# Optimization experiments

Hardware: AMD Instinct MI355X
Metric: run time of the kernel (lower is better)

The kernel has to match this reference:

```python
import jax, jax.numpy as jnp
import numpy as np

EPS = 1e-5

def _layer_norm(y, w, b):
    mu = y.mean(-1, keepdims=True)
    var = jnp.mean((y - mu) ** 2, axis=-1, keepdims=True)
    return (y - mu) * jax.lax.rsqrt(var + EPS) * w + b


def setup_inputs() -> dict:
    key = jax.random.key(0)
    ks = jax.random.split(key, 8)
    B, D, H, W = 1, 96, 96, 96
    N, R, K = 16, 6, 4
    x = jax.random.normal(ks[0], (B, D, H, W), jnp.float32)
    x_proj_weight = jax.random.normal(ks[1], (K, R + 2 * N, D), jnp.float32) * 0.05
    dt_projs_weight = jax.random.normal(ks[2], (K, D, R), jnp.float32) * 0.1
    dt_projs_bias = jax.random.normal(ks[3], (K, D), jnp.float32) * 0.1
    A_logs = jax.random.normal(ks[4], (K * D, N), jnp.float32)
    Ds = jax.random.normal(ks[5], (K * D,), jnp.float32) * 0.1
    ln_w = jnp.ones((D,), jnp.float32)
    ln_b = jnp.zeros((D,), jnp.float32)
    return {"x": x, "x_proj_weight": x_proj_weight, "dt_projs_weight": dt_projs_weight,
            "dt_projs_bias": dt_projs_bias, "A_logs": A_logs, "Ds": Ds,
            "ln_w": ln_w, "ln_b": ln_b}


def reference(x, x_proj_weight, dt_projs_weight, dt_projs_bias, A_logs, Ds, ln_w, ln_b):
    B, D, H, W = x.shape
    L = H * W
    K = x_proj_weight.shape[0]            # 4 scan directions
    N = A_logs.shape[1]                   # d_state
    R = dt_projs_weight.shape[2]          # dt_rank

    # ---- CrossScan: 4 directional flattenings -> xs [B, K, D, L]
    xs0 = x.reshape(B, D, L)
    xs1 = jnp.swapaxes(x, 2, 3).reshape(B, D, L)
    xs = jnp.stack([xs0, xs1, xs0[:, :, ::-1], xs1[:, :, ::-1]], axis=1)

    # ---- input-dependent projections
    x_dbl = jnp.einsum('bkdl,kcd->bkcl', xs, x_proj_weight)    # [B,K,R+2N,L]
    dts = x_dbl[:, :, :R]
    Bs = x_dbl[:, :, R:R + N]                                  # [B,K,N,L]
    Cs = x_dbl[:, :, R + N:]                                   # [B,K,N,L]
    dts = jnp.einsum('bkrl,kdr->bkdl', dts, dt_projs_weight)   # [B,K,D,L]

    # ---- selective scan (S6), delta_softplus=True, fp32
    delta = jax.nn.softplus(dts + dt_projs_bias[None, :, :, None])   # [B,K,D,L]
    A = -jnp.exp(A_logs).reshape(K, D, N)                             # [K,D,N]
    dA = jnp.exp(jnp.einsum('bkdl,kdn->bkdln', delta, A))             # [B,K,D,L,N]
    dBu = jnp.einsum('bkdl,bknl,bkdl->bkdln', delta, Bs, xs)          # delta*B*u

    def combine(c1, c2):
        a1, b1 = c1
        a2, b2 = c2
        return a1 * a2, a2 * b1 + b2

    _, h = jax.lax.associative_scan(combine, (dA, dBu), axis=3)       # h_t over L

    y = jnp.einsum('bkdln,bknl->bkdl', h, Cs)
    y = y + xs * Ds.reshape(K, D)[None, :, :, None]                   # [B,K,D,L]

    # ---- CrossMerge: undo the 4 directional scans and sum
    ys = y[:, 0:2] + y[:, 2:4, :, ::-1]                               # [B,2,D,L]
    ym = ys[:, 0] + jnp.swapaxes(ys[:, 1].reshape(B, D, W, H), 2, 3).reshape(B, D, L)

    # ---- out_norm (LayerNorm over D) and reshape to [B,H,W,D]
    yout = jnp.swapaxes(ym, 1, 2)                                     # [B,L,D]
    yout = _layer_norm(yout, ln_w, ln_b).reshape(B, H, W, D)
    return yout.astype(x.dtype)
```

## Files before the change

### kernel.cpp

```cpp
#include <hip/hip_runtime.h>
#include <math.h>

constexpr int cD = 96, cL = 9216, cK = 4;
constexpr int CL = 36, NCH = 256;
constexpr long cDL = (long)cD * cL;
constexpr float LOG2E = 1.44269504088896f;

constexpr long OFF_XT    = 0;
constexpr long OFF_DELTA = OFF_XT    + cDL;
constexpr long OFF_BC    = OFF_DELTA + 4L*cDL;
constexpr long OFF_Y     = OFF_BC    + 4L*cL*32;
constexpr long OFF_YT    = OFF_Y     + 4L*cDL;

__device__ __forceinline__ float4 a2prep(float4 v) {
    return make_float4(-LOG2E * exp2f(LOG2E * v.x), -LOG2E * exp2f(LOG2E * v.y),
                       -LOG2E * exp2f(LOG2E * v.z), -LOG2E * exp2f(LOG2E * v.w));
}
template<int C>
__device__ __forceinline__ float qperm(float v) {
    return __int_as_float(__builtin_amdgcn_mov_dpp(__float_as_int(v), C, 0xf, 0xf, true));
}

__global__ __launch_bounds__(256) void kT(const float* __restrict__ x,
                                          float* __restrict__ xT) {
    __shared__ float t[32][33];
    const int h0 = blockIdx.x * 32, w0 = blockIdx.y * 32, d = blockIdx.z;
    const float* xd = x + (long)d * cL;
    float* xtd = xT + (long)d * cL;
    for (int o = threadIdx.x; o < 1024; o += 256) {
        int i = o >> 5, j = o & 31;
        t[i][j] = xd[(h0 + i) * 96 + w0 + j];
    }
    __syncthreads();
    for (int o = threadIdx.x; o < 1024; o += 256) {
        int i = o >> 5, j = o & 31;
        xtd[(w0 + i) * 96 + h0 + j] = t[j][i];
    }
}

__global__ __launch_bounds__(256) void kA(const float* __restrict__ x,
                                          const float* __restrict__ xT,
                                          const float* __restrict__ xpw,
                                          const float* __restrict__ dtw,
                                          const float* __restrict__ dtb,
                                          float* __restrict__ delta,
                                          float* __restrict__ BC) {
    __shared__ float xs[96][64];
    __shared__ float xdbl[38][65];
    __shared__ float dtw_l[96 * 6];
    __shared__ float dtb_l[96];
    const int p0 = blockIdx.x * 64;
    const int k  = blockIdx.y;
    const int tid = threadIdx.x;
    const float* src = (k & 1) ? xT : x;

    for (int o = tid; o < 96 * 64; o += 256) {
        int dd = o >> 6, pp = o & 63;
        xs[dd][pp] = src[(long)dd * cL + p0 + pp];
    }
    for (int o = tid; o < 96 * 6; o += 256) dtw_l[o] = dtw[k * 96 * 6 + o];
    if (tid < 96) dtb_l[tid] = dtb[k * 96 + tid];
    __syncthreads();

    const int lane = tid & 63;
    const int c0 = __builtin_amdgcn_readfirstlane((tid >> 6) * 10);
    const float* wk = xpw + (long)k * 38 * 96;
    float acc[10];
    #pragma unroll
    for (int i = 0; i < 10; ++i) acc[i] = 0.f;
    #pragma unroll 4
    for (int dd = 0; dd < 96; ++dd) {
        float xv = xs[dd][lane];
        #pragma unroll
        for (int i = 0; i < 10; ++i) {
            int c = c0 + i; c = c > 37 ? 37 : c;
            acc[i] = fmaf(xv, wk[c * 96 + dd], acc[i]);
        }
    }
    #pragma unroll
    for (int i = 0; i < 10; ++i) {
        int c = c0 + i; c = c > 37 ? 37 : c;
        xdbl[c][lane] = acc[i];
    }
    __syncthreads();

    for (int o = tid; o < 64 * 16; o += 256) {
        int n = o & 15, pp = o >> 4;
        int P = p0 + pp;
        int q = (k < 2) ? P : (9215 - P);
        int ch = q / 36, j = q - ch * 36;
        long idx = (((long)k * 36 + j) * 256 + ch) * 32 + n;
        BC[idx]      = xdbl[6 + n][pp];
        BC[idx + 16] = xdbl[22 + n][pp];
    }
    for (int o = tid; o < 96 * 64; o += 256) {
        int dd = o >> 6, pp = o & 63;
        float s = dtb_l[dd];
        #pragma unroll
        for (int r = 0; r < 6; ++r) s = fmaf(xdbl[r][pp], dtw_l[dd * 6 + r], s);
        float sp = fmaxf(s, 0.f) + __logf(1.f + __expf(-fabsf(s)));
        delta[((long)(k * 96 + dd)) * cL + p0 + pp] = sp;
    }
}

__global__ __launch_bounds__(1024, 2) void kS(const float* __restrict__ x,
                                              const float* __restrict__ xT,
                                              const float* __restrict__ delta,
                                              const float* __restrict__ BC,
                                              const float* __restrict__ Alog,
                                              const float* __restrict__ Dsv,
                                              float* __restrict__ y) {
    __shared__ float lp[NCH][16];
    __shared__ float ls[NCH][16];
    float* gpf = &lp[0][0];
    const int tid = threadIdx.x;
    const int seq = blockIdx.x;
    const int k = seq / 96, d = seq % 96, rev = k >> 1;
    const int n0 = (tid & 3) * 4, ch = tid >> 2;
    const int r = tid & 3;
    const int q0 = rev ? (9215 - ch * CL) : ch * CL;

    const float4 a2 = a2prep(*(const float4*)(Alog + (long)seq * 16 + n0));
    const float Dv = Dsv[seq];
    const float* dB = delta + (long)seq * cL + q0;
    const float* xB = ((k & 1) ? xT : x) + (long)d * cL + q0;
    const float* bcB = BC + (long)k * cL * 32 + (long)ch * 32 + n0;

    float4 h = make_float4(0.f, 0.f, 0.f, 0.f);
    float sdl = 0.f;
#define S1(DL, XV, OFF) { \
        float4 B = *(const float4*)(bcB + (OFF) * 8192); \
        float t = (DL) * (XV); sdl += (DL); \
        h.x = fmaf(exp2f((DL)*a2.x), h.x, t*B.x); \
        h.y = fmaf(exp2f((DL)*a2.y), h.y, t*B.y); \
        h.z = fmaf(exp2f((DL)*a2.z), h.z, t*B.z); \
        h.w = fmaf(exp2f((DL)*a2.w), h.w, t*B.w); }
    if (!rev) {
        #pragma unroll
        for (int g = 0; g < 9; ++g) {
            float4 d4 = *(const float4*)(dB + 4*g);
            float4 x4 = *(const float4*)(xB + 4*g);
            S1(d4.x, x4.x, 4*g)   S1(d4.y, x4.y, 4*g+1)
            S1(d4.z, x4.z, 4*g+2) S1(d4.w, x4.w, 4*g+3)
        }
    } else {
        #pragma unroll
        for (int g = 0; g < 9; ++g) {
            float4 d4 = *(const float4*)(dB - 4*g - 3);
            float4 x4 = *(const float4*)(xB - 4*g - 3);
            S1(d4.w, x4.w, 4*g)   S1(d4.z, x4.z, 4*g+1)
            S1(d4.y, x4.y, 4*g+2) S1(d4.x, x4.x, 4*g+3)
        }
    }
#undef S1
    *(float4*)&lp[ch][n0] = make_float4(exp2f(a2.x*sdl), exp2f(a2.y*sdl),
                                        exp2f(a2.z*sdl), exp2f(a2.w*sdl));
    *(float4*)&ls[ch][n0] = h;
    __syncthreads();

    const int sn = tid & 15, sg = tid >> 4;
    float LPe[4], LSe[4];
    {
        float P = 1.f, S = 0.f;
        #pragma unroll
        for (int i = 0; i < 4; ++i) {
            LPe[i] = P; LSe[i] = S;
            float p = lp[sg * 4 + i][sn], s = ls[sg * 4 + i][sn];
            S = fmaf(p, S, s); P = p * P;
        }
        __syncthreads();
        gpf[tid] = P; gpf[1024 + tid] = S;
    }
    __syncthreads();
    #pragma unroll
    for (int off = 1; off < 64; off <<= 1) {
        float pc = gpf[tid], sc = gpf[1024 + tid];
        float pn = pc, snn = sc;
        if (sg >= off) {
            pn  = pc * gpf[tid - off * 16];
            snn = fmaf(pc, gpf[1024 + tid - off * 16], sc);
        }
        __syncthreads();
        gpf[tid] = pn; gpf[1024 + tid] = snn;
        __syncthreads();
    }
    const float GS = (sg == 0) ? 0.f : gpf[1024 + tid - 16];
    #pragma unroll
    for (int i = 0; i < 4; ++i) ls[sg * 4 + i][sn] = fmaf(LPe[i], GS, LSe[i]);
    __syncthreads();

    h = *(float4*)&ls[ch][n0];
    float* yq = y + (long)seq * cL + ch * CL;
    float yhold = 0.f;
#define S2(DL, XV, SI, OFF) { \
        float4 B = *(const float4*)(bcB + (OFF) * 8192); \
        float4 C = *(const float4*)(bcB + (OFF) * 8192 + 16); \
        float t = (DL) * (XV); \
        h.x = fmaf(exp2f((DL)*a2.x), h.x, t*B.x); \
        h.y = fmaf(exp2f((DL)*a2.y), h.y, t*B.y); \
        h.z = fmaf(exp2f((DL)*a2.z), h.z, t*B.z); \
        h.w = fmaf(exp2f((DL)*a2.w), h.w, t*B.w); \
        float pv = fmaf(h.x, C.x, fmaf(h.y, C.y, fmaf(h.z, C.z, h.w * C.w))); \
        pv += qperm<0xB1>(pv); \
        pv += qperm<0x4E>(pv); \
        if ((SI) == r) yhold = fmaf(Dv, (XV), pv); }
    if (!rev) {
        #pragma unroll
        for (int g = 0; g < 9; ++g) {
            float4 d4 = *(const float4*)(dB + 4*g);
            float4 x4 = *(const float4*)(xB + 4*g);
            S2(d4.x, x4.x, 0, 4*g)   S2(d4.y, x4.y, 1, 4*g+1)
            S2(d4.z, x4.z, 2, 4*g+2) S2(d4.w, x4.w, 3, 4*g+3)
            yq[4*g + r] = yhold;
        }
    } else {
        #pragma unroll
        for (int g = 0; g < 9; ++g) {
            float4 d4 = *(const float4*)(dB - 4*g - 3);
            float4 x4 = *(const float4*)(xB - 4*g - 3);
            S2(d4.w, x4.w, 0, 4*g)   S2(d4.z, x4.z, 1, 4*g+1)
            S2(d4.y, x4.y, 2, 4*g+2) S2(d4.x, x4.x, 3, 4*g+3)
            yq[4*g + r] = yhold;
        }
    }
#undef S2
}

__global__ __launch_bounds__(256) void kU(const float* __restrict__ Y,
                                          float* __restrict__ YT) {
    __shared__ float t[32][33];
    const int i0 = blockIdx.x * 32, j0 = blockIdx.y * 32;
    const int z = blockIdx.z;
    const int arr = z / 96, d = z % 96;
    const float* src = Y + (1 + 2 * arr) * cDL + (long)d * cL;
    float* dst = YT + (long)arr * cDL + (long)d * cL;
    for (int o = threadIdx.x; o < 1024; o += 256) {
        int i = o >> 5, j = o & 31;
        t[i][j] = src[(i0 + i) * 96 + j0 + j];
    }
    __syncthreads();
    for (int o = threadIdx.x; o < 1024; o += 256) {
        int i = o >> 5, j = o & 31;
        dst[(j0 + i) * 96 + i0 + j] = t[j][i];
    }
}

__global__ __launch_bounds__(256) void kE(const float* __restrict__ Y,
                                          const float* __restrict__ YT,
                                          const float* __restrict__ lnw,
                                          const float* __restrict__ lnb,
                                          float* __restrict__ out) {
    __shared__ float vs[96][36];
    __shared__ float red[8][32], red2[8][32];
    __shared__ float MU[32], RS[32];
    const int tid = threadIdx.x;
    const int p0 = blockIdx.x * 32;

    for (int o = tid; o < 96 * 8; o += 256) {
        int dd = o >> 3, j = o & 7;
        const float* r0 = Y + (long)dd * cL + p0;
        const float* r1 = YT + (long)dd * cL + p0;
        const float* r2 = Y + 2 * cDL + (long)dd * cL;
        const float* r3 = YT + cDL + (long)dd * cL;
        float4 a = ((const float4*)r0)[j];
        float4 b = ((const float4*)r1)[j];
        float4 c = *(const float4*)(r2 + 9212 - p0 - 4 * j);
        float4 e = *(const float4*)(r3 + 9212 - p0 - 4 * j);
        *(float4*)&vs[dd][4 * j] = make_float4(a.x + b.x + c.w + e.w,
                                               a.y + b.y + c.z + e.z,
                                               a.z + b.z + c.y + e.y,
                                               a.w + b.w + c.x + e.x);
    }
    __syncthreads();

    const int p = tid & 31, part = tid >> 5;
    float s = 0.f, s2 = 0.f;
    for (int dd = part * 12; dd < part * 12 + 12; ++dd) {
        float v = vs[dd][p];
        s += v; s2 = fmaf(v, v, s2);
    }
    red[part][p] = s; red2[part][p] = s2;
    __syncthreads();
    if (tid < 32) {
        float S = 0.f, S2 = 0.f;
        #pragma unroll
        for (int q = 0; q < 8; ++q) { S += red[q][tid]; S2 += red2[q][tid]; }
        float m = S * (1.f / 96.f);
        MU[tid] = m;
        RS[tid] = rsqrtf(S2 * (1.f / 96.f) - m * m + 1e-5f);
    }
    __syncthreads();
    for (int o = tid; o < 32 * 96; o += 256) {
        int pl = o / 96, dd = o - pl * 96;
        out[(long)(p0 + pl) * 96 + dd] = (vs[dd][pl] - MU[pl]) * RS[pl] * lnw[dd] + lnb[dd];
    }
}

extern "C" void kernel_launch(void* const* d_in, const int* in_sizes, int n_in,
                              void* d_out, int out_size, void* d_ws, size_t ws_size,
                              hipStream_t stream) {
    const float* x    = (const float*)d_in[0];
    const float* xpw  = (const float*)d_in[1];
    const float* dtw  = (const float*)d_in[2];
    const float* dtb  = (const float*)d_in[3];
    const float* Alog = (const float*)d_in[4];
    const float* Dsv  = (const float*)d_in[5];
    const float* lnw  = (const float*)d_in[6];
    const float* lnb  = (const float*)d_in[7];
    float* ws = (float*)d_ws;

    float* xT    = ws + OFF_XT;
    float* delta = ws + OFF_DELTA;
    float* BC    = ws + OFF_BC;
    float* y     = ws + OFF_Y;
    float* yT    = ws + OFF_YT;
    float* out   = (float*)d_out;

    kT<<<dim3(3, 3, 96), 256, 0, stream>>>(x, xT);
    kA<<<dim3(144, 4), 256, 0, stream>>>(x, xT, xpw, dtw, dtb, delta, BC);
    kS<<<cK * cD, 1024, 0, stream>>>(x, xT, delta, BC, Alog, Dsv, y);
    kU<<<dim3(3, 3, 192), 256, 0, stream>>>(y, yT);
    kE<<<288, 256, 0, stream>>>(y, yT, lnw, lnb, out);
}
```

Measured before the change: 113.6 us.

## Split chunked selective scan into two kernels with half-sequence blocks

Replaces the single 1024-thread scan kernel with two kernels. The first computes per-chunk decay products and partial states into global buffers. The second reloads all chunk summaries, redoes the cross-chunk prefix, and runs the output pass, each block covering half of a sequence's chunks. The point is more, smaller blocks (768 × 512 threads with higher occupancy bounds) to better fill the GPU. The B/C buffer is also reordered so each group of four timesteps sits contiguously per chunk. The costs are an extra launch, a global round trip for chunk summaries, and a prefix computed redundantly by both halves.

```diff
diff --git a/kernel.cpp b/kernel.cpp
--- a/kernel.cpp
+++ b/kernel.cpp
@@ -11,6 +11,8 @@
 constexpr long OFF_BC    = OFF_DELTA + 4L*cDL;
 constexpr long OFF_Y     = OFF_BC    + 4L*cL*32;
 constexpr long OFF_YT    = OFF_Y     + 4L*cDL;
+constexpr long OFF_PG    = OFF_YT    + 2L*cDL;
+constexpr long OFF_SG    = OFF_PG    + 384L*256*16;
 
 __device__ __forceinline__ float4 a2prep(float4 v) {
     return make_float4(-LOG2E * exp2f(LOG2E * v.x), -LOG2E * exp2f(LOG2E * v.y),
@@ -89,7 +91,8 @@
         int P = p0 + pp;
         int q = (k < 2) ? P : (9215 - P);
         int ch = q / 36, j = q - ch * 36;
-        long idx = (((long)k * 36 + j) * 256 + ch) * 32 + n;
+        int g = j >> 2, r = j & 3;
+        long idx = ((((long)k * 9 + g) * 256 + ch) * 4 + r) * 32 + n;
         BC[idx]      = xdbl[6 + n][pp];
         BC[idx + 16] = xdbl[22 + n][pp];
     }
@@ -103,98 +106,126 @@
     }
 }
 
-__global__ __launch_bounds__(1024, 2) void kS(const float* __restrict__ x,
+__global__ __launch_bounds__(512, 6) void kS1(const float* __restrict__ x,
+                                              const float* __restrict__ xT,
+                                              const float* __restrict__ delta,
+                                              const float* __restrict__ BC,
+                                              const float* __restrict__ Alog,
+                                              float* __restrict__ Pg,
+                                              float* __restrict__ Sg) {
+    const int tid = threadIdx.x;
+    const int n0 = (tid & 3) * 4, chl = tid >> 2;
+    const int hb = blockIdx.x & 1, seq = blockIdx.x >> 1;
+    const int k = seq / 96, d = seq % 96, rev = k >> 1;
+    const int ch = hb * 128 + chl;
+    const int q0 = ch * CL;
+
+    const float4 a2 = a2prep(*(const float4*)(Alog + (long)seq * 16 + n0));
+    const float* dRow = delta + (long)seq * cL;
+    const float* xRow = ((k & 1) ? xT : x) + (long)d * cL;
+    const float* bc0 = BC + ((long)k * 9 * 256 * 4 + (long)ch * 4) * 32 + n0;
+
+    float4 h = make_float4(0.f, 0.f, 0.f, 0.f);
+    float sdl = 0.f;
+#define ST(DL, XV, BPTR, ROFF) { \
+        float4 B = *(const float4*)((BPTR) + (ROFF) * 32); \
+        float t = (DL) * (XV); sdl += (DL); \
+        h.x = fmaf(exp2f((DL)*a2.x), h.x, t*B.x); \
+        h.y = fmaf(exp2f((DL)*a2.y), h.y, t*B.y); \
+        h.z = fmaf(exp2f((DL)*a2.z), h.z, t*B.z); \
+        h.w = fmaf(exp2f((DL)*a2.w), h.w, t*B.w); }
+    #pragma unroll
+    for (int g = 0; g < 9; ++g) {
+        const float* bg = bc0 + (long)g * 32768;
+        if (!rev) {
+            float4 d4 = *(const float4*)(dRow + q0 + 4 * g);
+            float4 x4 = *(const float4*)(xRow + q0 + 4 * g);
+            ST(d4.x, x4.x, bg, 0) ST(d4.y, x4.y, bg, 1)
+            ST(d4.z, x4.z, bg, 2) ST(d4.w, x4.w, bg, 3)
+        } else {
+            float4 d4 = *(const float4*)(dRow + 9212 - q0 - 4 * g);
+            float4 x4 = *(const float4*)(xRow + 9212 - q0 - 4 * g);
+            ST(d4.w, x4.w, bg, 0) ST(d4.z, x4.z, bg, 1)
+            ST(d4.y, x4.y, bg, 2) ST(d4.x, x4.x, bg, 3)
+        }
+    }
+#undef ST
+    long o = ((long)seq * NCH + ch) * 16 + n0;
+    *(float4*)(Pg + o) = make_float4(exp2f(a2.x*sdl), exp2f(a2.y*sdl),
+                                     exp2f(a2.z*sdl), exp2f(a2.w*sdl));
+    *(float4*)(Sg + o) = h;
+}
+
+__global__ __launch_bounds__(512, 6) void kS2(const float* __restrict__ x,
                                               const float* __restrict__ xT,
                                               const float* __restrict__ delta,
                                               const float* __restrict__ BC,
                                               const float* __restrict__ Alog,
                                               const float* __restrict__ Dsv,
+                                              const float* __restrict__ Pg,
+                                              const float* __restrict__ Sg,
                                               float* __restrict__ y) {
     __shared__ float lp[NCH][16];
     __shared__ float ls[NCH][16];
     float* gpf = &lp[0][0];
     const int tid = threadIdx.x;
-    const int seq = blockIdx.x;
+    const int hb = blockIdx.x & 1, seq = blockIdx.x >> 1;
     const int k = seq / 96, d = seq % 96, rev = k >> 1;
-    const int n0 = (tid & 3) * 4, ch = tid >> 2;
-    const int r = tid & 3;
-    const int q0 = rev ? (9215 - ch * CL) : ch * CL;
-
-    const float4 a2 = a2prep(*(const float4*)(Alog + (long)seq * 16 + n0));
-    const float Dv = Dsv[seq];
-    const float* dB = delta + (long)seq * cL + q0;
-    const float* xB = ((k & 1) ? xT : x) + (long)d * cL + q0;
-    const float* bcB = BC + (long)k * cL * 32 + (long)ch * 32 + n0;
-
-    float4 h = make_float4(0.f, 0.f, 0.f, 0.f);
-    float sdl = 0.f;
-#define S1(DL, XV, OFF) { \
-        float4 B = *(const float4*)(bcB + (OFF) * 8192); \
-        float t = (DL) * (XV); sdl += (DL); \
-        h.x = fmaf(exp2f((DL)*a2.x), h.x, t*B.x); \
-        h.y = fmaf(exp2f((DL)*a2.y), h.y, t*B.y); \
-        h.z = fmaf(exp2f((DL)*a2.z), h.z, t*B.z); \
-        h.w = fmaf(exp2f((DL)*a2.w), h.w, t*B.w); }
-    if (!rev) {
-        #pragma unroll
-        for (int g = 0; g < 9; ++g) {
-            float4 d4 = *(const float4*)(dB + 4*g);
-            float4 x4 = *(const float4*)(xB + 4*g);
-            S1(d4.x, x4.x, 4*g)   S1(d4.y, x4.y, 4*g+1)
-            S1(d4.z, x4.z, 4*g+2) S1(d4.w, x4.w, 4*g+3)
-        }
-    } else {
-        #pragma unroll
-        for (int g = 0; g < 9; ++g) {
-            float4 d4 = *(const float4*)(dB - 4*g - 3);
-            float4 x4 = *(const float4*)(xB - 4*g - 3);
-            S1(d4.w, x4.w, 4*g)   S1(d4.z, x4.z, 4*g+1)
-            S1(d4.y, x4.y, 4*g+2) S1(d4.x, x4.x, 4*g+3)
-        }
-    }
-#undef S1
-    *(float4*)&lp[ch][n0] = make_float4(exp2f(a2.x*sdl), exp2f(a2.y*sdl),
-                                        exp2f(a2.z*sdl), exp2f(a2.w*sdl));
-    *(float4*)&ls[ch][n0] = h;
+
+    #pragma unroll
+    for (int i = 0; i < 8; ++i) {
+        ((float*)lp)[tid + i * 512] = Pg[(long)seq * 4096 + tid + i * 512];
+        ((float*)ls)[tid + i * 512] = Sg[(long)seq * 4096 + tid + i * 512];
+    }
     __syncthreads();
 
     const int sn = tid & 15, sg = tid >> 4;
-    float LPe[4], LSe[4];
+    float LPe[8], LSe[8];
     {
         float P = 1.f, S = 0.f;
         #pragma unroll
-        for (int i = 0; i < 4; ++i) {
+        for (int i = 0; i < 8; ++i) {
             LPe[i] = P; LSe[i] = S;
-            float p = lp[sg * 4 + i][sn], s = ls[sg * 4 + i][sn];
+            float p = lp[sg * 8 + i][sn], s = ls[sg * 8 + i][sn];
             S = fmaf(p, S, s); P = p * P;
         }
         __syncthreads();
-        gpf[tid] = P; gpf[1024 + tid] = S;
-    }
-    __syncthreads();
-    #pragma unroll
-    for (int off = 1; off < 64; off <<= 1) {
-        float pc = gpf[tid], sc = gpf[1024 + tid];
+        gpf[tid] = P; gpf[512 + tid] = S;
+    }
+    __syncthreads();
+    #pragma unroll
+    for (int off = 1; off < 32; off <<= 1) {
+        float pc = gpf[tid], sc = gpf[512 + tid];
         float pn = pc, snn = sc;
         if (sg >= off) {
             pn  = pc * gpf[tid - off * 16];
-            snn = fmaf(pc, gpf[1024 + tid - off * 16], sc);
+            snn = fmaf(pc, gpf[512 + tid - off * 16], sc);
         }
         __syncthreads();
-        gpf[tid] = pn; gpf[1024 + tid] = snn;
+        gpf[tid] = pn; gpf[512 + tid] = snn;
         __syncthreads();
     }
-    const float GS = (sg == 0) ? 0.f : gpf[1024 + tid - 16];
-    #pragma unroll
-    for (int i = 0; i < 4; ++i) ls[sg * 4 + i][sn] = fmaf(LPe[i], GS, LSe[i]);
-    __syncthreads();
-
-    h = *(float4*)&ls[ch][n0];
-    float* yq = y + (long)seq * cL + ch * CL;
+    const float GS = (sg == 0) ? 0.f : gpf[512 + tid - 16];
+    #pragma unroll
+    for (int i = 0; i < 8; ++i) ls[sg * 8 + i][sn] = fmaf(LPe[i], GS, LSe[i]);
+    __syncthreads();
+
+    const int n0 = (tid & 3) * 4, chl = tid >> 2;
+    const int r = tid & 3;
+    const int ch = hb * 128 + chl;
+    const int q0 = ch * CL;
+    const float4 a2 = a2prep(*(const float4*)(Alog + (long)seq * 16 + n0));
+    const float Dv = Dsv[seq];
+    const float* dRow = delta + (long)seq * cL;
+    const float* xRow = ((k & 1) ? xT : x) + (long)d * cL;
+    const float* bc0 = BC + ((long)k * 9 * 256 * 4 + (long)ch * 4) * 32 + n0;
+    float4 h = *(float4*)&ls[ch][n0];
+    float* yq = y + (long)seq * cL + q0;
     float yhold = 0.f;
-#define S2(DL, XV, SI, OFF) { \
-        float4 B = *(const float4*)(bcB + (OFF) * 8192); \
-        float4 C = *(const float4*)(bcB + (OFF) * 8192 + 16); \
+
+#define ST(DL, XV, BPTR, ROFF, SI) { \
+        float4 B = *(const float4*)((BPTR) + (ROFF) * 32); \
+        float4 C = *(const float4*)((BPTR) + (ROFF) * 32 + 16); \
         float t = (DL) * (XV); \
         h.x = fmaf(exp2f((DL)*a2.x), h.x, t*B.x); \
         h.y = fmaf(exp2f((DL)*a2.y), h.y, t*B.y); \
@@ -204,26 +235,23 @@
         pv += qperm<0xB1>(pv); \
         pv += qperm<0x4E>(pv); \
         if ((SI) == r) yhold = fmaf(Dv, (XV), pv); }
-    if (!rev) {
-        #pragma unroll
-        for (int g = 0; g < 9; ++g) {
-            float4 d4 = *(const float4*)(dB + 4*g);
-            float4 x4 = *(const float4*)(xB + 4*g);
-            S2(d4.x, x4.x, 0, 4*g)   S2(d4.y, x4.y, 1, 4*g+1)
-            S2(d4.z, x4.z, 2, 4*g+2) S2(d4.w, x4.w, 3, 4*g+3)
-            yq[4*g + r] = yhold;
-        }
-    } else {
-        #pragma unroll
-        for (int g = 0; g < 9; ++g) {
-            float4 d4 = *(const float4*)(dB - 4*g - 3);
-            float4 x4 = *(const float4*)(xB - 4*g - 3);
-            S2(d4.w, x4.w, 0, 4*g)   S2(d4.z, x4.z, 1, 4*g+1)
-            S2(d4.y, x4.y, 2, 4*g+2) S2(d4.x, x4.x, 3, 4*g+3)
-            yq[4*g + r] = yhold;
-        }
-    }
-#undef S2
+    #pragma unroll
+    for (int g = 0; g < 9; ++g) {
+        const float* bg = bc0 + (long)g * 32768;
+        if (!rev) {
+            float4 d4 = *(const float4*)(dRow + q0 + 4 * g);
+            float4 x4 = *(const float4*)(xRow + q0 + 4 * g);
+            ST(d4.x, x4.x, bg, 0, 0) ST(d4.y, x4.y, bg, 1, 1)
+            ST(d4.z, x4.z, bg, 2, 2) ST(d4.w, x4.w, bg, 3, 3)
+        } else {
+            float4 d4 = *(const float4*)(dRow + 9212 - q0 - 4 * g);
+            float4 x4 = *(const float4*)(xRow + 9212 - q0 - 4 * g);
+            ST(d4.w, x4.w, bg, 0, 0) ST(d4.z, x4.z, bg, 1, 1)
+            ST(d4.y, x4.y, bg, 2, 2) ST(d4.x, x4.x, bg, 3, 3)
+        }
+        yq[4 * g + r] = yhold;
+    }
+#undef ST
 }
 
 __global__ __launch_bounds__(256) void kU(const float* __restrict__ Y,
@@ -314,11 +342,14 @@
     float* BC    = ws + OFF_BC;
     float* y     = ws + OFF_Y;
     float* yT    = ws + OFF_YT;
+    float* Pg    = ws + OFF_PG;
+    float* Sg    = ws + OFF_SG;
     float* out   = (float*)d_out;
 
     kT<<<dim3(3, 3, 96), 256, 0, stream>>>(x, xT);
     kA<<<dim3(144, 4), 256, 0, stream>>>(x, xT, xpw, dtw, dtb, delta, BC);
-    kS<<<cK * cD, 1024, 0, stream>>>(x, xT, delta, BC, Alog, Dsv, y);
+    kS1<<<768, 512, 0, stream>>>(x, xT, delta, BC, Alog, Pg, Sg);
+    kS2<<<768, 512, 0, stream>>>(x, xT, delta, BC, Alog, Dsv, Pg, Sg, y);
     kU<<<dim3(3, 3, 192), 256, 0, stream>>>(y, yT);
     kE<<<288, 256, 0, stream>>>(y, yT, lnw, lnb, out);
 }
```

New measurement: 111.4 us. 1.02x faster.
